# Kernel optimization log

Hardware: AMD Instinct MI355X
Metric: run time of the kernel (lower is better)

## Reference

```python
import jax, jax.numpy as jnp
import numpy as np


def setup_inputs() -> dict:
    key = jax.random.key(0)
    k1, k2, k3 = jax.random.split(key, 3)
    B, C, H, W = 16, 19, 512, 512
    predictions = jax.random.normal(k1, (B, C, H, W), dtype=jnp.float32)
    targets = jax.random.randint(k2, (B, H, W), 0, C, dtype=jnp.int32)
    label_mask = (jax.random.uniform(k3, (B, H, W)) < 0.02).astype(jnp.float32)
    return {"predictions": predictions, "targets": targets, "label_mask": label_mask}


def reference(predictions, targets, label_mask):
    B, C, H, W = predictions.shape
    t = targets.reshape(-1)                      # [N]
    m = label_mask.reshape(-1)                   # [N]

    # --- class weights: inverse frequency over labeled pixels ---
    # single scatter-add pass replaces the per-class loop
    counts = jax.ops.segment_sum(m, t, num_segments=C)  # [C]
    total = counts.sum()
    w = total / (counts + 1e-6)
    w = w / w.sum() * C
    class_weights = jnp.where(total > 0, w, jnp.ones((C,), dtype=predictions.dtype))

    # --- weighted partial cross-entropy ---
    logits = predictions.transpose(0, 2, 3, 1).reshape(-1, C)  # [N, C]
    log_probs = jax.nn.log_softmax(logits, axis=-1)
    nll = -jnp.take_along_axis(log_probs, t[:, None], axis=1)[:, 0]  # [N]
    loss_per_pixel = nll * class_weights[t]
    masked_loss = loss_per_pixel * m

    num_labeled = m.sum()
    return jnp.where(num_labeled > 0, masked_loss.sum() / num_labeled, masked_loss.sum())
```

## Files before the change

kernel.cpp:

```cpp
#include <hip/hip_runtime.h>
#include <math.h>


constexpr int C      = 19;
constexpr int HWp    = 512 * 512;
constexpr int LOG2HW = 18;
constexpr int NPIX   = 16 * HWp;
constexpr int PIXB   = 4096;
constexpr int ABLK   = NPIX / PIXB;
constexpr int V4B    = PIXB / 4;

__global__ __launch_bounds__(256) void wpce_compact(
        const int4* __restrict__ tgt4, const float4* __restrict__ msk4,
        unsigned* __restrict__ list, int* __restrict__ gcnt, int cap) {
    __shared__ unsigned ent[PIXB];
    __shared__ int sCnt, sBase;
    const int tid = threadIdx.x;
    if (tid == 0) sCnt = 0;
    __syncthreads();

    const int base_v = blockIdx.x * V4B;
#pragma unroll
    for (int it = 0; it < V4B / 256; ++it) {
        const int v = base_v + it * 256 + tid;
        const int4   t = tgt4[v];
        const float4 m = msk4[v];
        const unsigned i0 = (unsigned)v * 4u;
        if (m.x != 0.f) ent[atomicAdd(&sCnt, 1)] = (i0    ) | ((unsigned)t.x << 22);
        if (m.y != 0.f) ent[atomicAdd(&sCnt, 1)] = (i0 + 1) | ((unsigned)t.y << 22);
        if (m.z != 0.f) ent[atomicAdd(&sCnt, 1)] = (i0 + 2) | ((unsigned)t.z << 22);
        if (m.w != 0.f) ent[atomicAdd(&sCnt, 1)] = (i0 + 3) | ((unsigned)t.w << 22);
    }
    __syncthreads();
    if (tid == 0) sBase = atomicAdd(gcnt, sCnt);
    __syncthreads();
    const int n = sCnt, b = sBase;
    for (int i = tid; i < n; i += 256) {
        const int pos = b + i;
        if (pos < cap) list[pos] = ent[i];
    }
}

__global__ __launch_bounds__(256) void wpce_gather(
        const float* __restrict__ pred, const unsigned* __restrict__ list,
        const int* __restrict__ gcnt, float* __restrict__ ws, int cap) {
    __shared__ float sS[C], sCt[C];
    const int tid = threadIdx.x;
    if (tid < C) { sS[tid] = 0.f; sCt[tid] = 0.f; }
    __syncthreads();

    const int n = min(*gcnt, cap);
    const int stride = gridDim.x * blockDim.x;
    for (int j = blockIdx.x * blockDim.x + tid; j < n; j += stride) {
        const unsigned e = list[j];
        const int idx = (int)(e & 0x3FFFFFu);
        const int t   = (int)(e >> 22);
        const float* p = pred + (((size_t)(idx >> LOG2HW) * C) << LOG2HW)
                              + (idx & (HWp - 1));
        float x[C];
        float mx = -3.4e38f, xt = 0.f;
#pragma unroll
        for (int c = 0; c < C; ++c) {
            const float v = p[(size_t)c << LOG2HW];
            x[c] = v;
            mx = fmaxf(mx, v);
            xt = (c == t) ? v : xt;
        }
        float se = 0.f;
#pragma unroll
        for (int c = 0; c < C; ++c) se += __expf(x[c] - mx);
        const float nll = mx + __logf(se) - xt;
        atomicAdd(&sS[t], nll);
        atomicAdd(&sCt[t], 1.f);
    }
    __syncthreads();
    if (tid < C && (sS[tid] != 0.f || sCt[tid] != 0.f)) {
        atomicAdd(&ws[tid],     sS[tid]);
        atomicAdd(&ws[C + tid], sCt[tid]);
    }
}

__global__ void wpce_fin(const float* __restrict__ ws, float* __restrict__ out) {
    const int l = threadIdx.x;
    float S   = (l < C) ? ws[l]     : 0.f;
    float cnt = (l < C) ? ws[C + l] : 0.f;

    float total = cnt;
    for (int o = 1; o < 64; o <<= 1) total += __shfl_xor(total, o);

    float w = (l < C) ? total / (cnt + 1e-6f) : 0.f;
    float sw = w;
    for (int o = 1; o < 64; o <<= 1) sw += __shfl_xor(sw, o);

    float loss = (l < C) ? (w / sw * (float)C) * S : 0.f;
    for (int o = 1; o < 64; o <<= 1) loss += __shfl_xor(loss, o);

    if (l == 0) out[0] = (total > 0.f) ? loss / total : 0.f;
}

extern "C" void kernel_launch(void* const* d_in, const int* in_sizes, int n_in,
                              void* d_out, int out_size, void* d_ws, size_t ws_size,
                              hipStream_t stream) {
    const float* pred = (const float*)d_in[0];
    const int*   tgt  = (const int*)  d_in[1];
    const float* msk  = (const float*)d_in[2];

    float*    ws   = (float*)d_ws;
    int*      gcnt = (int*)((char*)d_ws + 192);
    unsigned* list = (unsigned*)((char*)d_ws + 1024);
    const long capl = ((long)ws_size - 1024) / 4;
    const int  cap  = (capl > NPIX) ? NPIX : (int)capl;

    hipMemsetAsync(d_ws, 0, 256, stream);

    wpce_compact<<<ABLK, 256, 0, stream>>>((const int4*)tgt, (const float4*)msk,
                                           list, gcnt, cap);
    wpce_gather<<<512, 256, 0, stream>>>(pred, list, gcnt, ws, cap);
    wpce_fin<<<1, 64, 0, stream>>>(ws, (float*)d_out);
}
```

Measured before the change: 55.44 us.

## Fuse compaction and gather into one kernel using per-block shared list

```diff
diff --git a/kernel.cpp b/kernel.cpp
--- a/kernel.cpp
+++ b/kernel.cpp
@@ -6,22 +6,25 @@
 constexpr int HWp    = 512 * 512;
 constexpr int LOG2HW = 18;
 constexpr int NPIX   = 16 * HWp;
-constexpr int PIXB   = 4096;
-constexpr int ABLK   = NPIX / PIXB;
-constexpr int V4B    = PIXB / 4;
+constexpr int WPIX   = 4096;
+constexpr int ABLK   = NPIX / WPIX;
+constexpr int ITERS  = WPIX / 4 / 256;
 
-__global__ __launch_bounds__(256) void wpce_compact(
+__global__ __launch_bounds__(256) void wpce_fused(
+        const float* __restrict__ pred,
         const int4* __restrict__ tgt4, const float4* __restrict__ msk4,
-        unsigned* __restrict__ list, int* __restrict__ gcnt, int cap) {
-    __shared__ unsigned ent[PIXB];
-    __shared__ int sCnt, sBase;
+        float* __restrict__ ws) {
+    __shared__ unsigned ent[WPIX];
+    __shared__ int sCnt;
+    __shared__ float sS[C], sCt[C];
     const int tid = threadIdx.x;
     if (tid == 0) sCnt = 0;
+    if (tid < C) { sS[tid] = 0.f; sCt[tid] = 0.f; }
     __syncthreads();
 
-    const int base_v = blockIdx.x * V4B;
+    const int base_v = blockIdx.x * (WPIX / 4);
 #pragma unroll
-    for (int it = 0; it < V4B / 256; ++it) {
+    for (int it = 0; it < ITERS; ++it) {
         const int v = base_v + it * 256 + tid;
         const int4   t = tgt4[v];
         const float4 m = msk4[v];
@@ -32,27 +35,10 @@
         if (m.w != 0.f) ent[atomicAdd(&sCnt, 1)] = (i0 + 3) | ((unsigned)t.w << 22);
     }
     __syncthreads();
-    if (tid == 0) sBase = atomicAdd(gcnt, sCnt);
-    __syncthreads();
-    const int n = sCnt, b = sBase;
-    for (int i = tid; i < n; i += 256) {
-        const int pos = b + i;
-        if (pos < cap) list[pos] = ent[i];
-    }
-}
 
-__global__ __launch_bounds__(256) void wpce_gather(
-        const float* __restrict__ pred, const unsigned* __restrict__ list,
-        const int* __restrict__ gcnt, float* __restrict__ ws, int cap) {
-    __shared__ float sS[C], sCt[C];
-    const int tid = threadIdx.x;
-    if (tid < C) { sS[tid] = 0.f; sCt[tid] = 0.f; }
-    __syncthreads();
-
-    const int n = min(*gcnt, cap);
-    const int stride = gridDim.x * blockDim.x;
-    for (int j = blockIdx.x * blockDim.x + tid; j < n; j += stride) {
-        const unsigned e = list[j];
+    const int n = sCnt;
+    for (int j = tid; j < n; j += 256) {
+        const unsigned e = ent[j];
         const int idx = (int)(e & 0x3FFFFFu);
         const int t   = (int)(e >> 22);
         const float* p = pred + (((size_t)(idx >> LOG2HW) * C) << LOG2HW)
@@ -74,6 +60,7 @@
         atomicAdd(&sCt[t], 1.f);
     }
     __syncthreads();
+
     if (tid < C && (sS[tid] != 0.f || sCt[tid] != 0.f)) {
         atomicAdd(&ws[tid],     sS[tid]);
         atomicAdd(&ws[C + tid], sCt[tid]);
@@ -104,17 +91,11 @@
     const float* pred = (const float*)d_in[0];
     const int*   tgt  = (const int*)  d_in[1];
     const float* msk  = (const float*)d_in[2];
+    float* ws = (float*)d_ws;
 
-    float*    ws   = (float*)d_ws;
-    int*      gcnt = (int*)((char*)d_ws + 192);
-    unsigned* list = (unsigned*)((char*)d_ws + 1024);
-    const long capl = ((long)ws_size - 1024) / 4;
-    const int  cap  = (capl > NPIX) ? NPIX : (int)capl;
+    hipMemsetAsync(d_ws, 0, 2 * C * sizeof(float), stream);
 
-    hipMemsetAsync(d_ws, 0, 256, stream);
-
-    wpce_compact<<<ABLK, 256, 0, stream>>>((const int4*)tgt, (const float4*)msk,
-                                           list, gcnt, cap);
-    wpce_gather<<<512, 256, 0, stream>>>(pred, list, gcnt, ws, cap);
+    wpce_fused<<<ABLK, 256, 0, stream>>>(pred, (const int4*)tgt,
+                                         (const float4*)msk, ws);
     wpce_fin<<<1, 64, 0, stream>>>(ws, (float*)d_out);
 }
```

New measurement: 58.69 us. 5.9% more time.
